# Kernel tuning notes

Measured on AMD Instinct MI355X. Metric: run time of the kernel, lower is better.

The kernel has to match this reference:

```python
import jax, jax.numpy as jnp
import numpy as np

NUM_HEADS = 16


def setup_inputs() -> dict:
    key = jax.random.key(0)
    ks = jax.random.split(key, 6)
    B, S, H = 4, 2048, 1024
    x = jax.random.normal(ks[0], (B, S, H), dtype=jnp.float32)
    mask = jax.random.randint(ks[1], (B, 1, 1, S), 0, 2, dtype=jnp.int32)
    scale = 1.0 / np.sqrt(H)
    Wq = jax.random.normal(ks[2], (H, H), dtype=jnp.float32) * scale
    Wk = jax.random.normal(ks[3], (H, H), dtype=jnp.float32) * scale
    Wv = jax.random.normal(ks[4], (H, H), dtype=jnp.float32) * scale
    Wo = jax.random.normal(ks[5], (H, H), dtype=jnp.float32) * scale
    bo = jnp.zeros((H,), dtype=jnp.float32)
    return {"x": x, "mask": mask, "Wq": Wq, "Wk": Wk, "Wv": Wv, "Wo": Wo, "bo": bo}


def reference(x, mask, Wq, Wk, Wv, Wo, bo):
    B, S, H = x.shape
    nh = NUM_HEADS
    dk = H // nh

    def split_heads(t):  # (B,S,H) -> (B,nh,S,dk)
        return t.reshape(B, S, nh, dk).transpose(0, 2, 1, 3)

    # torch Linear: y = x @ W.T (q/k/v bias-free)
    q = split_heads(x @ Wq.T)
    k = split_heads(x @ Wk.T)
    v = split_heads(x @ Wv.T)

    scores = jnp.einsum('bhqd,bhkd->bhqk', q, k) / jnp.sqrt(jnp.float32(dk))
    scores = jnp.where(mask == 0, jnp.float32(-1e9), scores)
    attn = jax.nn.softmax(scores, axis=-1)  # dropout is identity in eval mode
    out = jnp.einsum('bhqk,bhkd->bhqd', attn, v)
    out = out.transpose(0, 2, 1, 3).reshape(B, S, H)
    return out @ Wo.T + bo
```

## Files before the change

kernel.cpp:

```cpp
#include <hip/hip_runtime.h>
#include <hip/hip_bf16.h>

typedef __attribute__((ext_vector_type(8))) short sh8;
typedef __attribute__((ext_vector_type(4))) float f32x4;

#define MFMA16(a, b, c) __builtin_amdgcn_mfma_f32_16x16x32_bf16((a), (b), (c), 0, 0, 0)

__device__ __forceinline__ unsigned short f2bf(float f) {
    return (unsigned short)((__float_as_uint(f) + 0x8000u) >> 16);
}
__device__ __forceinline__ unsigned int pack2bf(float lo, float hi) {
    unsigned int ul = __float_as_uint(lo) + 0x8000u;
    unsigned int uh = __float_as_uint(hi) + 0x8000u;
    return __builtin_amdgcn_perm(uh, ul, 0x07060302u);
}
__device__ __forceinline__ float redmax_hi(float x) {
    x = fmaxf(x, __shfl_xor(x, 16, 64));
    return fmaxf(x, __shfl_xor(x, 32, 64));
}
__device__ __forceinline__ float redsum_hi(float x) {
    x += __shfl_xor(x, 16, 64);
    return x + __shfl_xor(x, 32, 64);
}
__device__ __forceinline__ void gload_lds16(const void* g, void* l) {
    __builtin_amdgcn_global_load_lds(
        (const __attribute__((address_space(1))) unsigned int*)g,
        (__attribute__((address_space(3))) unsigned int*)l, 16, 0, 0);
}

__global__ __launch_bounds__(256) void cvt_x_k(
    const float* __restrict__ src, unsigned short* __restrict__ dst, int n4)
{
    int i = blockIdx.x * 256 + threadIdx.x;
    int stride = gridDim.x * 256;
    for (; i < n4; i += stride) {
        float4 v = ((const float4*)src)[i];
        uint2 h = { pack2bf(v.x, v.y), pack2bf(v.z, v.w) };
        ((uint2*)dst)[i] = h;
    }
}
__global__ __launch_bounds__(256) void cvt_w_k(
    const float* __restrict__ Wq, const float* __restrict__ Wk,
    const float* __restrict__ Wv, const float* __restrict__ Wo,
    unsigned short* __restrict__ wbf)
{
    int i = blockIdx.x * 256 + threadIdx.x;
    int seg = i >> 18;
    int off = i & 0x3FFFF;
    const float* s = (seg < 2) ? ((seg == 0) ? Wq : Wk) : ((seg == 2) ? Wv : Wo);
    float4 v = ((const float4*)s)[off];
    uint2 h = { pack2bf(v.x, v.y), pack2bf(v.z, v.w) };
    ((uint2*)wbf)[i] = h;
}

__global__ __launch_bounds__(64) void compact_k(
    const int* __restrict__ mask, int* __restrict__ idx, int* __restrict__ cnt)
{
    const int b = blockIdx.x, l = threadIdx.x;
    const int* mb = mask + b * 2048;
    int base = 0;
    for (int i = 0; i < 32; ++i) {
        int m = mb[i * 64 + l];
        unsigned long long bal = __ballot(m != 0);
        int pre = __popcll(bal & ((1ull << l) - 1ull));
        if (m) idx[b * 2048 + base + pre] = i * 64 + l;
        base += (int)__popcll(bal);
    }
    if (base == 0) {
        for (int i = l; i < 2048; i += 64) idx[b * 2048 + i] = i;
        base = 2048;
    }
    if (l == 0) cnt[b] = base;
}

__global__ __launch_bounds__(256) void gemm_qkv_k(
    const unsigned short* __restrict__ xbf,
    const unsigned short* __restrict__ wbf,
    unsigned short* __restrict__ qkv)
{
    __shared__ unsigned short As[128][32];
    __shared__ unsigned short Bs[128][32];
    const int tid = threadIdx.x;
    const int l = tid & 63, w = tid >> 6;
    const int wr = w >> 1, wc = w & 1;
    const long row0 = (long)blockIdx.y * 128;
    const int col0 = blockIdx.x * 128;

    f32x4 acc[4][4] = {};
    const int fr = l & 15, hi = l >> 4;

    const int sr = tid >> 2;
    const int sc = (tid & 3) * 8;
    const unsigned short* ga = &xbf[(row0 + sr) * 1024 + sc];
    const unsigned short* gb = &wbf[(long)(col0 + sr) * 1024 + sc];
    unsigned short* la = &As[w * 16][0];
    unsigned short* lb = &Bs[w * 16][0];

    for (int k0 = 0; k0 < 1024; k0 += 32) {
        __syncthreads();
        gload_lds16(ga + k0, la);
        gload_lds16(ga + 64 * 1024 + k0, la + 64 * 32);
        gload_lds16(gb + k0, lb);
        gload_lds16(gb + 64 * 1024 + k0, lb + 64 * 32);
        __syncthreads();

        sh8 af[4], bf[4];
#pragma unroll
        for (int i = 0; i < 4; ++i) {
            af[i] = *(const sh8*)&As[wr * 64 + i * 16 + fr][hi * 8];
            bf[i] = *(const sh8*)&Bs[wc * 64 + i * 16 + fr][hi * 8];
        }
#pragma unroll
        for (int i = 0; i < 4; ++i)
#pragma unroll
            for (int j = 0; j < 4; ++j)
                acc[i][j] = MFMA16(af[i], bf[j], acc[i][j]);
    }

    const float scale = (col0 < 1024) ? 0.1803368801f : 1.0f;
    const int rg = hi * 4, cg = l & 15;
#pragma unroll
    for (int i = 0; i < 4; ++i)
#pragma unroll
        for (int j = 0; j < 4; ++j) {
            long gr = row0 + wr * 64 + i * 16 + rg;
            int gc = col0 + wc * 64 + j * 16 + cg;
#pragma unroll
            for (int r = 0; r < 4; ++r)
                qkv[(gr + r) * 3072 + gc] = f2bf(acc[i][j][r] * scale);
        }
}

__global__ __launch_bounds__(256) void attn_k(
    const unsigned short* __restrict__ qkv, const int* __restrict__ idx,
    const int* __restrict__ cnt, unsigned short* __restrict__ ao, int b0)
{
    __shared__ unsigned short Kl[64][64];
    __shared__ unsigned short Vt[64][64];
    __shared__ float biasf[64];
    __shared__ unsigned short Pl[4][16][72];

    const int tid = threadIdx.x;
    const int l = tid & 63, w = tid >> 6;
    const int fr = l & 15, hi = l >> 4;

    int nwg = gridDim.x;
    int wgid = ((nwg & 7) == 0) ? ((blockIdx.x & 7) * (nwg >> 3) + (blockIdx.x >> 3))
                                : blockIdx.x;
    const int qb = wgid & 31;
    const int h  = (wgid >> 5) & 15;
    const int b  = wgid >> 9;
    const int q0 = qb * 64;
    const long base = (long)b * 2048;

    const int* idxb = idx + (size_t)(b0 + b) * 2048;
    const int nc = cnt[b0 + b];
    const int nt = (nc + 63) >> 6;

    sh8 qf0, qf1;
    {
        const unsigned short* qp = &qkv[(base + q0 + w * 16 + fr) * 3072 + h * 64 + hi * 8];
        qf0 = *(const sh8*)qp;
        qf1 = *(const sh8*)(qp + 32);
    }

    f32x4 acc[4] = {};
    float mrow = -1e30f;
    float lrow = 0.f;

    const int rK = tid >> 3, cc = tid & 7;
    const int kv2 = tid >> 3, dc = tid & 7;

    uint4 k0r, k1r, v0r, v1r;
    {
        int ik0 = idxb[min(rK, nc - 1)];
        int ik1 = idxb[min(rK + 32, nc - 1)];
        int iv0 = idxb[min(2 * kv2, nc - 1)];
        int iv1 = idxb[min(2 * kv2 + 1, nc - 1)];
        k0r = *(const uint4*)&qkv[(base + ik0) * 3072 + 1024 + h * 64 + cc * 8];
        k1r = *(const uint4*)&qkv[(base + ik1) * 3072 + 1024 + h * 64 + cc * 8];
        v0r = *(const uint4*)&qkv[(base + iv0) * 3072 + 2048 + h * 64 + dc * 8];
        v1r = *(const uint4*)&qkv[(base + iv1) * 3072 + 2048 + h * 64 + dc * 8];
    }

    for (int t = 0; t < nt; ++t) {
        __syncthreads();
        *(uint4*)&Kl[rK][(cc ^ (rK & 7)) * 8] = k0r;
        {
            int r2 = rK + 32;
            *(uint4*)&Kl[r2][(cc ^ (r2 & 7)) * 8] = k1r;
        }
        {
            unsigned int w0[4] = { v0r.x, v0r.y, v0r.z, v0r.w };
            unsigned int w1[4] = { v1r.x, v1r.y, v1r.z, v1r.w };
            int cc2 = kv2 >> 2, pos = (2 * kv2) & 7;
#pragma unroll
            for (int jj = 0; jj < 4; ++jj) {
                int de = dc * 8 + 2 * jj;
                unsigned int pe = (w0[jj] & 0xffffu) | (w1[jj] << 16);
                unsigned int po = (w0[jj] >> 16) | (w1[jj] & 0xffff0000u);
                int fde = (2 * jj) ^ dc;
                int fdo = (2 * jj + 1) ^ dc;
                *(unsigned int*)&Vt[de][((cc2 ^ fde) * 8) + pos] = pe;
                *(unsigned int*)&Vt[de + 1][((cc2 ^ fdo) * 8) + pos] = po;
            }
        }
        if (tid < 64) biasf[tid] = (t * 64 + tid < nc) ? 0.0f : -1e9f;
        __syncthreads();

        if (t + 1 < nt) {
            int s0 = (t + 1) * 64;
            int ik0 = idxb[min(s0 + rK, nc - 1)];
            int ik1 = idxb[min(s0 + rK + 32, nc - 1)];
            int iv0 = idxb[min(s0 + 2 * kv2, nc - 1)];
            int iv1 = idxb[min(s0 + 2 * kv2 + 1, nc - 1)];
            k0r = *(const uint4*)&qkv[(base + ik0) * 3072 + 1024 + h * 64 + cc * 8];
            k1r = *(const uint4*)&qkv[(base + ik1) * 3072 + 1024 + h * 64 + cc * 8];
            v0r = *(const uint4*)&qkv[(base + iv0) * 3072 + 2048 + h * 64 + dc * 8];
            v1r = *(const uint4*)&qkv[(base + iv1) * 3072 + 2048 + h * 64 + dc * 8];
        }

        sh8 kf[4][2];
#pragma unroll
        for (int tt = 0; tt < 4; ++tt) {
            const unsigned short* kp = &Kl[tt * 16 + fr][0];
#pragma unroll
            for (int c = 0; c < 2; ++c)
                kf[tt][c] = *(const sh8*)&kp[((4 * c + hi) ^ (fr & 7)) * 8];
        }

        f32x4 s[4] = {};
        __builtin_amdgcn_s_setprio(1);
#pragma unroll
        for (int tt = 0; tt < 4; ++tt) {
            s[tt] = MFMA16(kf[tt][0], qf0, s[tt]);
            s[tt] = MFMA16(kf[tt][1], qf1, s[tt]);
        }
        __builtin_amdgcn_s_setprio(0);
#pragma unroll
        for (int tt = 0; tt < 4; ++tt)
            s[tt] += *(const f32x4*)&biasf[tt * 16 + 4 * hi];

        float pm = s[0][0];
#pragma unroll
        for (int tt = 0; tt < 4; ++tt)
#pragma unroll
            for (int r = 0; r < 4; ++r) pm = fmaxf(pm, s[tt][r]);
        pm = redmax_hi(pm);

        if (!__all(pm <= mrow)) {
            float mn = fmaxf(mrow, pm);
            float scl = __builtin_amdgcn_exp2f(mrow - mn);
            lrow *= scl;
#pragma unroll
            for (int df = 0; df < 4; ++df) acc[df] *= scl;
            mrow = mn;
        }

        float ps = 0.f;
#pragma unroll
        for (int tt = 0; tt < 4; ++tt)
#pragma unroll
            for (int r = 0; r < 4; ++r) {
                float p = __builtin_amdgcn_exp2f(s[tt][r] - mrow);
                s[tt][r] = p;
                ps += p;
            }
        lrow += redsum_hi(ps);

#pragma unroll
        for (int tt = 0; tt < 4; ++tt) {
            uint2 pw = { pack2bf(s[tt][0], s[tt][1]), pack2bf(s[tt][2], s[tt][3]) };
            *(uint2*)&Pl[w][fr][tt * 16 + hi * 4] = pw;
        }

#pragma unroll
        for (int c = 0; c < 2; ++c) {
            sh8 pa = *(const sh8*)&Pl[w][fr][c * 32 + hi * 8];
            __builtin_amdgcn_s_setprio(1);
#pragma unroll
            for (int df = 0; df < 4; ++df) {
                int d = df * 16 + fr;
                int fd = (d & 7) ^ (d >> 3);
                sh8 vfr = *(const sh8*)&Vt[d][((4 * c + hi) ^ fd) * 8];
                acc[df] = MFMA16(vfr, pa, acc[df]);
            }
            __builtin_amdgcn_s_setprio(0);
        }
    }

    {
        float inv = 1.0f / lrow;
        long qr = base + q0 + w * 16 + fr;
        unsigned short* op = &ao[qr * 1024 + h * 64];
#pragma unroll
        for (int df = 0; df < 4; ++df) {
            f32x4 o = acc[df];
            uint2 ow = { pack2bf(o[0] * inv, o[1] * inv), pack2bf(o[2] * inv, o[3] * inv) };
            *(uint2*)&op[df * 16 + hi * 4] = ow;
        }
    }
}

__global__ __launch_bounds__(256) void gemm_out_k(
    const unsigned short* __restrict__ ao, const unsigned short* __restrict__ wob,
    const float* __restrict__ bo, float* __restrict__ out)
{
    __shared__ unsigned short As[128][32];
    __shared__ unsigned short Bs[128][32];
    const int tid = threadIdx.x;
    const int l = tid & 63, w = tid >> 6;
    const int wr = w >> 1, wc = w & 1;
    const long row0 = (long)blockIdx.y * 128;
    const int col0 = blockIdx.x * 128;

    f32x4 acc[4][4] = {};
    const int fr = l & 15, hi = l >> 4;

    const int sr = tid >> 2;
    const int sc = (tid & 3) * 8;
    const unsigned short* ga = &ao[(row0 + sr) * 1024 + sc];
    const unsigned short* gb = &wob[(long)(col0 + sr) * 1024 + sc];
    unsigned short* la = &As[w * 16][0];
    unsigned short* lb = &Bs[w * 16][0];

    for (int k0 = 0; k0 < 1024; k0 += 32) {
        __syncthreads();
        gload_lds16(ga + k0, la);
        gload_lds16(ga + 64 * 1024 + k0, la + 64 * 32);
        gload_lds16(gb + k0, lb);
        gload_lds16(gb + 64 * 1024 + k0, lb + 64 * 32);
        __syncthreads();

        sh8 af[4], bf[4];
#pragma unroll
        for (int i = 0; i < 4; ++i) {
            af[i] = *(const sh8*)&As[wr * 64 + i * 16 + fr][hi * 8];
            bf[i] = *(const sh8*)&Bs[wc * 64 + i * 16 + fr][hi * 8];
        }
#pragma unroll
        for (int i = 0; i < 4; ++i)
#pragma unroll
            for (int j = 0; j < 4; ++j)
                acc[i][j] = MFMA16(af[i], bf[j], acc[i][j]);
    }

    const int rg = hi * 4, cg = l & 15;
#pragma unroll
    for (int i = 0; i < 4; ++i)
#pragma unroll
        for (int j = 0; j < 4; ++j) {
            long gr = row0 + wr * 64 + i * 16 + rg;
            int gc = col0 + wc * 64 + j * 16 + cg;
            float bb = bo[gc];
#pragma unroll
            for (int r = 0; r < 4; ++r)
                out[(gr + r) * 1024 + gc] = acc[i][j][r] + bb;
        }
}

extern "C" void kernel_launch(void* const* d_in, const int* in_sizes, int n_in,
                              void* d_out, int out_size, void* d_ws, size_t ws_size,
                              hipStream_t stream) {
    const float* x    = (const float*)d_in[0];
    const int*   mask = (const int*)d_in[1];
    const float* Wq   = (const float*)d_in[2];
    const float* Wk   = (const float*)d_in[3];
    const float* Wv   = (const float*)d_in[4];
    const float* Wo   = (const float*)d_in[5];
    const float* bo   = (const float*)d_in[6];
    float* out = (float*)d_out;

    const size_t wbf_bytes = (size_t)4096 * 1024 * 2;
    const size_t idx_bytes = (size_t)4 * 2048 * 4 + 64;
    const size_t xbf_per_b = (size_t)2048 * 1024 * 2;
    const size_t qkv_per_b = (size_t)2048 * 3072 * 2;
    const size_t ao_per_b  = (size_t)2048 * 1024 * 2;
    const size_t per_b = xbf_per_b + qkv_per_b + ao_per_b;

    size_t fixed = wbf_bytes + idx_bytes;
    size_t avail = (ws_size > fixed) ? (ws_size - fixed) : 0;
    int bchunk = (avail >= per_b) ? (int)(avail / per_b) : 1;
    if (bchunk > 4) bchunk = 4;

    char* p = (char*)d_ws;
    unsigned short* wbf = (unsigned short*)p;            p += wbf_bytes;
    int* idxp = (int*)p;                                 p += (size_t)4 * 2048 * 4;
    int* cntp = (int*)p;                                 p += 64;
    unsigned short* xbf = (unsigned short*)p;            p += (size_t)bchunk * xbf_per_b;
    unsigned short* qkv = (unsigned short*)p;            p += (size_t)bchunk * qkv_per_b;
    unsigned short* ao  = (unsigned short*)p;

    cvt_w_k<<<4096, 256, 0, stream>>>(Wq, Wk, Wv, Wo, wbf);
    compact_k<<<4, 64, 0, stream>>>(mask, idxp, cntp);

    for (int b0 = 0; b0 < 4; b0 += bchunk) {
        int bc = (4 - b0 < bchunk) ? (4 - b0) : bchunk;
        cvt_x_k<<<2048, 256, 0, stream>>>(
            x + (size_t)b0 * 2048 * 1024, xbf, bc * 524288);
        gemm_qkv_k<<<dim3(24, bc * 16), 256, 0, stream>>>(xbf, wbf, qkv);
        attn_k<<<dim3(512 * bc), 256, 0, stream>>>(qkv, idxp, cntp, ao, b0);
        gemm_out_k<<<dim3(8, bc * 16), 256, 0, stream>>>(
            ao, wbf + (size_t)3072 * 1024, bo, out + (size_t)b0 * 2048 * 1024);
    }
}
```

Measured before the change: 214.9 us.

## Pre-gather masked K/V rows into a compact buffer and use direct-to-LDS K loads

Adds a gather kernel that copies the K and V rows selected by the mask index list into a contiguous per-batch buffer, padded to 64-row tiles. The attention kernel then streams K with global-to-LDS loads at a fixed stride and reads V with plain strided loads, with no per-tile index lookups. The aim is to remove indirect, scattered gathers and their address-calculation latency from the attention inner loop. In exchange it adds an extra kernel launch, an extra read and write of K/V, and more workspace, which can reduce the batch chunk size.

```diff
diff --git a/kernel.cpp b/kernel.cpp
--- a/kernel.cpp
+++ b/kernel.cpp
@@ -73,6 +73,27 @@
     if (l == 0) cnt[b] = base;
 }
 
+__global__ __launch_bounds__(256) void kvgather_k(
+    const unsigned short* __restrict__ qkv, const int* __restrict__ idx,
+    const int* __restrict__ cnt, unsigned short* __restrict__ Kc, int b0)
+{
+    const int b = blockIdx.z;
+    const int t = blockIdx.y;
+    const int z = blockIdx.x;
+    const int nc = cnt[b0 + b];
+    if (t * 64 >= ((nc + 63) & ~63)) return;
+    const int* idxb = idx + (size_t)(b0 + b) * 2048;
+    const int tid = threadIdx.x;
+    unsigned short* dst_b = Kc + (size_t)b * 2048 * 2048;
+#pragma unroll
+    for (int p = 0; p < 8; ++p) {
+        int row = t * 64 + z * 8 + p;
+        int src = idxb[min(row, nc - 1)];
+        uint4 v = *(const uint4*)&qkv[((size_t)b * 2048 + src) * 3072 + 1024 + tid * 8];
+        *(uint4*)&dst_b[(size_t)row * 2048 + tid * 8] = v;
+    }
+}
+
 __global__ __launch_bounds__(256) void gemm_qkv_k(
     const unsigned short* __restrict__ xbf,
     const unsigned short* __restrict__ wbf,
@@ -132,7 +153,7 @@
 }
 
 __global__ __launch_bounds__(256) void attn_k(
-    const unsigned short* __restrict__ qkv, const int* __restrict__ idx,
+    const unsigned short* __restrict__ qkv, const unsigned short* __restrict__ Kc,
     const int* __restrict__ cnt, unsigned short* __restrict__ ao, int b0)
 {
     __shared__ unsigned short Kl[64][64];
@@ -153,7 +174,6 @@
     const int q0 = qb * 64;
     const long base = (long)b * 2048;
 
-    const int* idxb = idx + (size_t)(b0 + b) * 2048;
     const int nc = cnt[b0 + b];
     const int nt = (nc + 63) >> 6;
 
@@ -168,28 +188,25 @@
     float mrow = -1e30f;
     float lrow = 0.f;
 
-    const int rK = tid >> 3, cc = tid & 7;
+    const long TS = 262144;
+    const char* kc_b = (const char*)Kc + (size_t)b * 2048 * 4096;
+
+    const int l8 = l >> 3, c8 = l & 7;
+    const char* ksrc = kc_b + (size_t)(w * 16 + l8) * 4096 + h * 128 + ((c8 ^ l8) * 16);
+    unsigned short* kdst0 = &Kl[w * 16][0];
+    unsigned short* kdst1 = &Kl[w * 16 + 8][0];
+
     const int kv2 = tid >> 3, dc = tid & 7;
-
-    uint4 k0r, k1r, v0r, v1r;
-    {
-        int ik0 = idxb[min(rK, nc - 1)];
-        int ik1 = idxb[min(rK + 32, nc - 1)];
-        int iv0 = idxb[min(2 * kv2, nc - 1)];
-        int iv1 = idxb[min(2 * kv2 + 1, nc - 1)];
-        k0r = *(const uint4*)&qkv[(base + ik0) * 3072 + 1024 + h * 64 + cc * 8];
-        k1r = *(const uint4*)&qkv[(base + ik1) * 3072 + 1024 + h * 64 + cc * 8];
-        v0r = *(const uint4*)&qkv[(base + iv0) * 3072 + 2048 + h * 64 + dc * 8];
-        v1r = *(const uint4*)&qkv[(base + iv1) * 3072 + 2048 + h * 64 + dc * 8];
-    }
+    const char* vp0 = kc_b + (size_t)(2 * kv2) * 4096 + 2048 + h * 128 + dc * 16;
+    uint4 v0r = *(const uint4*)vp0;
+    uint4 v1r = *(const uint4*)(vp0 + 4096);
+    vp0 += TS;
 
     for (int t = 0; t < nt; ++t) {
         __syncthreads();
-        *(uint4*)&Kl[rK][(cc ^ (rK & 7)) * 8] = k0r;
-        {
-            int r2 = rK + 32;
-            *(uint4*)&Kl[r2][(cc ^ (r2 & 7)) * 8] = k1r;
-        }
+        gload_lds16(ksrc, kdst0);
+        gload_lds16(ksrc + 8 * 4096, kdst1);
+        ksrc += TS;
         {
             unsigned int w0[4] = { v0r.x, v0r.y, v0r.z, v0r.w };
             unsigned int w1[4] = { v1r.x, v1r.y, v1r.z, v1r.w };
@@ -209,15 +226,9 @@
         __syncthreads();
 
         if (t + 1 < nt) {
-            int s0 = (t + 1) * 64;
-            int ik0 = idxb[min(s0 + rK, nc - 1)];
-            int ik1 = idxb[min(s0 + rK + 32, nc - 1)];
-            int iv0 = idxb[min(s0 + 2 * kv2, nc - 1)];
-            int iv1 = idxb[min(s0 + 2 * kv2 + 1, nc - 1)];
-            k0r = *(const uint4*)&qkv[(base + ik0) * 3072 + 1024 + h * 64 + cc * 8];
-            k1r = *(const uint4*)&qkv[(base + ik1) * 3072 + 1024 + h * 64 + cc * 8];
-            v0r = *(const uint4*)&qkv[(base + iv0) * 3072 + 2048 + h * 64 + dc * 8];
-            v1r = *(const uint4*)&qkv[(base + iv1) * 3072 + 2048 + h * 64 + dc * 8];
+            v0r = *(const uint4*)vp0;
+            v1r = *(const uint4*)(vp0 + 4096);
+            vp0 += TS;
         }
 
         sh8 kf[4][2];
@@ -376,7 +387,8 @@
     const size_t xbf_per_b = (size_t)2048 * 1024 * 2;
     const size_t qkv_per_b = (size_t)2048 * 3072 * 2;
     const size_t ao_per_b  = (size_t)2048 * 1024 * 2;
-    const size_t per_b = xbf_per_b + qkv_per_b + ao_per_b;
+    const size_t kc_per_b  = (size_t)2048 * 2048 * 2;
+    const size_t per_b = xbf_per_b + qkv_per_b + ao_per_b + kc_per_b;
 
     size_t fixed = wbf_bytes + idx_bytes;
     size_t avail = (ws_size > fixed) ? (ws_size - fixed) : 0;
@@ -389,7 +401,8 @@
     int* cntp = (int*)p;                                 p += 64;
     unsigned short* xbf = (unsigned short*)p;            p += (size_t)bchunk * xbf_per_b;
     unsigned short* qkv = (unsigned short*)p;            p += (size_t)bchunk * qkv_per_b;
-    unsigned short* ao  = (unsigned short*)p;
+    unsigned short* ao  = (unsigned short*)p;            p += (size_t)bchunk * ao_per_b;
+    unsigned short* Kc  = (unsigned short*)p;
 
     cvt_w_k<<<4096, 256, 0, stream>>>(Wq, Wk, Wv, Wo, wbf);
     compact_k<<<4, 64, 0, stream>>>(mask, idxp, cntp);
@@ -399,7 +412,8 @@
         cvt_x_k<<<2048, 256, 0, stream>>>(
             x + (size_t)b0 * 2048 * 1024, xbf, bc * 524288);
         gemm_qkv_k<<<dim3(24, bc * 16), 256, 0, stream>>>(xbf, wbf, qkv);
-        attn_k<<<dim3(512 * bc), 256, 0, stream>>>(qkv, idxp, cntp, ao, b0);
+        kvgather_k<<<dim3(8, 32, bc), 256, 0, stream>>>(qkv, idxp, cntp, Kc, b0);
+        attn_k<<<dim3(512 * bc), 256, 0, stream>>>(qkv, Kc, cntp, ao, b0);
         gemm_out_k<<<dim3(8, bc * 16), 256, 0, stream>>>(
             ao, wbf + (size_t)3072 * 1024, bo, out + (size_t)b0 * 2048 * 1024);
     }
```

Result: faster. 210.0 us (-2.3%).
